# Performance work log

Measured on AMD Instinct MI355X. Metric: run time of the kernel, lower is better.

## Reference

```python
import jax, jax.numpy as jnp
import numpy as np

NUM_HEADS = 16
QKV = 1024
OUT = 1024
HEAD_DIM = QKV // NUM_HEADS


def _rel_shift(x):
    # x: [b,h,q,k] -> Transformer-XL relative shift
    zero_pad = jnp.zeros(x.shape[:-1] + (1,), dtype=x.dtype)
    x_padded = jnp.concatenate([zero_pad, x], axis=-1)
    x_padded = x_padded.reshape(x.shape[:-2] + (x.shape[-1] + 1, x.shape[-2]))
    return x_padded[..., 1:, :].reshape(x.shape)


def setup_inputs() -> dict:
    key = jax.random.key(0)
    ks = jax.random.split(key, 12)
    B, Q, K, D = 2, 2048, 2048, 1024
    s = 0.02
    return {
        "inputs_kv": jax.random.normal(ks[0], (B, K, D), jnp.float32),
        "inputs_q": jax.random.normal(ks[1], (B, Q, D), jnp.float32),
        "pos_embed": jax.random.normal(ks[2], (K, D), jnp.float32),
        "Wq_w": jax.random.normal(ks[3], (D, QKV), jnp.float32) * s,
        "Wq_b": jnp.zeros((QKV,), jnp.float32),
        "Wk_w": jax.random.normal(ks[4], (D, QKV), jnp.float32) * s,
        "Wk_b": jnp.zeros((QKV,), jnp.float32),
        "Wv_w": jax.random.normal(ks[5], (D, QKV), jnp.float32) * s,
        "Wv_b": jnp.zeros((QKV,), jnp.float32),
        "Wr_w": jax.random.normal(ks[6], (D, QKV), jnp.float32) * s,  # no bias
        "r_w_bias": jax.random.normal(ks[7], (NUM_HEADS, HEAD_DIM), jnp.float32) * s,
        "r_r_bias": jax.random.normal(ks[8], (NUM_HEADS, HEAD_DIM), jnp.float32) * s,
        "Wo_w": jax.random.normal(ks[9], (QKV, OUT), jnp.float32) * s,
        "Wo_b": jnp.zeros((OUT,), jnp.float32),
    }


def reference(inputs_kv, inputs_q, pos_embed, Wq_w, Wq_b, Wk_w, Wk_b, Wv_w, Wv_b,
              Wr_w, r_w_bias, r_r_bias, Wo_w, Wo_b):
    B, Q, _ = inputs_q.shape
    K = inputs_kv.shape[1]
    H, hd = NUM_HEADS, HEAD_DIM
    scale = hd ** (-0.5)

    q = (inputs_q @ Wq_w + Wq_b).reshape(B, Q, H, hd)
    k = (inputs_kv @ Wk_w + Wk_b).reshape(B, K, H, hd)
    v = (inputs_kv @ Wv_w + Wv_b).reshape(B, K, H, hd)
    r = (pos_embed @ Wr_w).reshape(K, H, hd)

    # content bias: [b,h,1,k]; position bias: [b,h,q,k] with rel-shift
    content_bias = jnp.einsum('hd,bkhd->bhk', r_w_bias, k)[:, :, None, :] * scale
    position_bias = jnp.einsum('bqhd,khd->bhqk', q + r_r_bias, r) * scale
    position_bias = _rel_shift(position_bias)
    combined_bias = content_bias + position_bias

    # dot_product_attention with extra bias and scale
    scores = jnp.einsum('bqhd,bkhd->bhqk', q, k) * scale + combined_bias
    probs = jax.nn.softmax(scores, axis=-1)
    out = jnp.einsum('bhqk,bkhd->bqhd', probs, v)

    out = out.reshape(B, Q, H * hd)
    return out @ Wo_w + Wo_b
```

## Files before the change

kernel.cpp:

```cpp
#include <hip/hip_runtime.h>
#include <hip/hip_fp16.h>


typedef float  floatx4 __attribute__((ext_vector_type(4)));
typedef __bf16 bf16x8  __attribute__((ext_vector_type(8)));
typedef _Float16 f16x8 __attribute__((ext_vector_type(8)));
typedef _Float16 f16x4 __attribute__((ext_vector_type(4)));
typedef _Float16 f16x2 __attribute__((ext_vector_type(2)));

#define LSTR 40
#define SCL 0.18033688f

struct GP {
  const void* A;
  const __bf16* B;
  int lda, ldb, K;
  float* outF;
  __bf16* out1;
  const float* bias;
};

__global__ void __launch_bounds__(256) gemm_o(GP p) {
  __shared__ __align__(16) __bf16 lA[128 * 32];
  __shared__ __align__(16) __bf16 lB[128 * 32];
  const int t = threadIdx.x;
  const int wave = t >> 6, lane = t & 63;
  const int m0 = blockIdx.y * 128, n0 = blockIdx.x * 128;
  const __bf16* Ab = (const __bf16*)p.A;
  const __bf16* Bb = p.B;

  floatx4 acc[4][4];
#pragma unroll
  for (int i = 0; i < 4; i++)
#pragma unroll
    for (int j = 0; j < 4; j++) acc[i][j] = floatx4{0.f, 0.f, 0.f, 0.f};

  const int lr = lane & 15, lq = lane >> 4;
  const int wr = (wave >> 1) << 6, wc = (wave & 1) << 6;

  for (int kk = 0; kk < 1024; kk += 32) {
#pragma unroll
    for (int i = 0; i < 2; i++) {
      const int idx = (i << 8) + t;
      const int row = idx >> 2, ch = (idx & 3) << 3;
      *(bf16x8*)&lA[row * 32 + ch] = *(const bf16x8*)(Ab + (long)(m0 + row) * 1024 + kk + ch);
      *(bf16x8*)&lB[row * 32 + ch] = *(const bf16x8*)(Bb + (long)(n0 + row) * 1024 + kk + ch);
    }
    __syncthreads();
    bf16x8 aF[4], bF[4];
#pragma unroll
    for (int i = 0; i < 4; i++)
      aF[i] = *(bf16x8*)&lA[(wr + i * 16 + lr) * 32 + (lq << 3)];
#pragma unroll
    for (int i = 0; i < 4; i++)
      bF[i] = *(bf16x8*)&lB[(wc + i * 16 + lr) * 32 + (lq << 3)];
#pragma unroll
    for (int i = 0; i < 4; i++)
#pragma unroll
      for (int j = 0; j < 4; j++)
        acc[i][j] = __builtin_amdgcn_mfma_f32_16x16x32_bf16(aF[i], bF[j], acc[i][j], 0, 0, 0);
    __syncthreads();
  }
#pragma unroll
  for (int i = 0; i < 4; i++)
#pragma unroll
    for (int j = 0; j < 4; j++) {
      int col = n0 + wc + j * 16 + lr;
#pragma unroll
      for (int g = 0; g < 4; g++) {
        int rl = m0 + wr + i * 16 + (lq << 2) + g;
        p.outF[(long)rl * 1024 + col] = acc[i][j][g] + p.bias[col];
      }
    }
}

struct QPAll {
  const float *qin, *kvin, *pos;
  const __bf16 *qinb, *kvinb, *posb;
  const __bf16 *Wtq, *Wtk, *Wtv, *Wtr;
  const float *bq, *bk, *bv, *rrb;
  __bf16 *qb, *qrr, *kb, *rb;
  _Float16 *vt;
};

template<bool BF16A>
__global__ void __launch_bounds__(256) qkvr_k(QPAll p) {
  constexpr int AST = BF16A ? 32 : LSTR;
  __shared__ __align__(16) __bf16 lA[128 * AST];
  __shared__ __align__(16) __bf16 lB[128 * AST];
  const int jb = blockIdx.x;
  const int job = (jb >= 768) ? 3 : (jb >> 8);
  const int local = jb - ((job == 3) ? 768 : (job << 8));
  const int m0 = (local >> 3) * 128, n0 = (local & 7) * 128;

  const float* Af; const __bf16* Ab; const __bf16* B; const float* bias;
  if (job == 0)      { Af = p.qin;  Ab = p.qinb;  B = p.Wtq; bias = p.bq; }
  else if (job == 1) { Af = p.kvin; Ab = p.kvinb; B = p.Wtk; bias = p.bk; }
  else if (job == 2) { Af = p.kvin; Ab = p.kvinb; B = p.Wtv; bias = p.bv; }
  else               { Af = p.pos;  Ab = p.posb;  B = p.Wtr; bias = nullptr; }

  const int t = threadIdx.x;
  const int wave = t >> 6, lane = t & 63;
  const int srow = t >> 2, scol = (t & 3) << 3;

  floatx4 acc[4][4];
#pragma unroll
  for (int i = 0; i < 4; i++)
#pragma unroll
    for (int j = 0; j < 4; j++) acc[i][j] = floatx4{0.f, 0.f, 0.f, 0.f};

  const int lr = lane & 15, lq = lane >> 4;
  const int wr = (wave >> 1) << 6, wc = (wave & 1) << 6;

  for (int kk = 0; kk < 1024; kk += 32) {
    if constexpr (BF16A) {
#pragma unroll
      for (int i = 0; i < 2; i++) {
        const int idx = (i << 8) + t;
        const int row = idx >> 2, ch = (idx & 3) << 3;
        *(bf16x8*)&lA[row * 32 + ch] = *(const bf16x8*)(Ab + (long)(m0 + row) * 1024 + kk + ch);
        *(bf16x8*)&lB[row * 32 + ch] = *(const bf16x8*)(B + (long)(n0 + row) * 1024 + kk + ch);
      }
    } else {
#pragma unroll
      for (int h2 = 0; h2 < 2; h2++) {
        int r = srow + (h2 << 6);
        const float* ap = Af + (long)(m0 + r) * 1024 + kk + scol;
        float4 f0 = *(const float4*)ap;
        float4 f1 = *(const float4*)(ap + 4);
        bf16x8 o;
        o[0] = (__bf16)f0.x; o[1] = (__bf16)f0.y; o[2] = (__bf16)f0.z; o[3] = (__bf16)f0.w;
        o[4] = (__bf16)f1.x; o[5] = (__bf16)f1.y; o[6] = (__bf16)f1.z; o[7] = (__bf16)f1.w;
        *(bf16x8*)&lA[r * AST + scol] = o;
        const __bf16* bp = B + (long)(n0 + r) * 1024 + kk + scol;
        *(bf16x8*)&lB[r * AST + scol] = *(const bf16x8*)bp;
      }
    }
    __syncthreads();
    bf16x8 aF[4], bF[4];
#pragma unroll
    for (int i = 0; i < 4; i++)
      aF[i] = *(bf16x8*)&lA[(wr + i * 16 + lr) * AST + (lq << 3)];
#pragma unroll
    for (int i = 0; i < 4; i++)
      bF[i] = *(bf16x8*)&lB[(wc + i * 16 + lr) * AST + (lq << 3)];
#pragma unroll
    for (int i = 0; i < 4; i++)
#pragma unroll
      for (int j = 0; j < 4; j++)
        acc[i][j] = __builtin_amdgcn_mfma_f32_16x16x32_bf16(aF[i], bF[j], acc[i][j], 0, 0, 0);
    __syncthreads();
  }

#pragma unroll
  for (int i = 0; i < 4; i++)
#pragma unroll
    for (int j = 0; j < 4; j++) {
      int col = n0 + wc + j * 16 + lr;
#pragma unroll
      for (int g = 0; g < 4; g++) {
        int rl = m0 + wr + i * 16 + (lq << 2) + g;
        float val = acc[i][j][g];
        int hh = col >> 6, d = col & 63;
        if (job == 3) {
          long dst = (((long)hh * 2048 + rl) << 6) + d;
          p.rb[dst] = (__bf16)val;
        } else {
          int bb = rl >> 11, s = rl & 2047;
          float v = val + bias[col];
          if (job == 0) {
            long dst = (((long)(bb * 16 + hh) * 2048 + s) << 6) + d;
            p.qb[dst] = (__bf16)v;
            p.qrr[dst] = (__bf16)(v + p.rrb[col]);
          } else if (job == 1) {
            long dst = (((long)(bb * 16 + hh) * 2048 + s) << 6) + d;
            p.kb[dst] = (__bf16)v;
          } else {
            long dst = ((((long)(bb * 16 + hh)) << 6) + d) * 2048 + s;
            p.vt[dst] = (_Float16)v;
          }
        }
      }
    }
}

__global__ void __launch_bounds__(256) cb_k(const __bf16* kb, const float* rwb, float* cb) {
  long id = (long)blockIdx.x * 256 + threadIdx.x;
  int z = (int)(id >> 11);
  int j = (int)(id & 2047);
  int h = z & 15;
  const __bf16* kp = kb + (((long)z * 2048 + j) << 6);
  float s = 0.f;
#pragma unroll
  for (int c = 0; c < 8; c++) {
    bf16x8 kv = *(const bf16x8*)(kp + c * 8);
#pragma unroll
    for (int e = 0; e < 8; e++) s += rwb[h * 64 + c * 8 + e] * (float)kv[e];
  }
  cb[id] = s * SCL;
}

struct TRP {
  const float* src[5]; __bf16* dst[5];
  const float* csrc[3]; __bf16* cdst[3]; long clen[3];
};
__global__ void __launch_bounds__(256) tr_cvt_all(TRP p) {
  const int id = blockIdx.x;
  if (id >= 1280) {
    const int cj = (id - 1280) >> 8;
    const int cbk = (id - 1280) & 255;
    const float* s = p.csrc[cj];
    __bf16* d = p.cdst[cj];
    const long n = p.clen[cj];
    for (long i = ((long)cbk * 256 + threadIdx.x) * 8; i < n; i += (long)256 * 256 * 8) {
      float4 f0 = *(const float4*)(s + i);
      float4 f1 = *(const float4*)(s + i + 4);
      bf16x8 o;
      o[0] = (__bf16)f0.x; o[1] = (__bf16)f0.y; o[2] = (__bf16)f0.z; o[3] = (__bf16)f0.w;
      o[4] = (__bf16)f1.x; o[5] = (__bf16)f1.y; o[6] = (__bf16)f1.z; o[7] = (__bf16)f1.w;
      *(bf16x8*)(d + i) = o;
    }
    return;
  }
  __shared__ float tile[64][65];
  const int which = id >> 8;
  const int local = id & 255;
  const int bx = local & 15, by = local >> 4;
  const float* src = p.src[which];
  __bf16* dst = p.dst[which];
  int tx = threadIdx.x & 63, ty = threadIdx.x >> 6;
#pragma unroll
  for (int r = ty; r < 64; r += 4)
    tile[r][tx] = src[(long)(by * 64 + r) * 1024 + bx * 64 + tx];
  __syncthreads();
#pragma unroll
  for (int r = ty; r < 64; r += 4)
    dst[(long)(bx * 64 + r) * 1024 + by * 64 + tx] = (__bf16)tile[tx][r];
}

#define QW 256
#define QSTR3 264
#define SM_ONE (32 * QSTR3 * 2)
#define FUSED_SMEM (2 * SM_ONE + 2048)

__global__ void __launch_bounds__(256, 4) fused_k(const __bf16* __restrict__ qb,
                                                  const __bf16* __restrict__ qrr,
                                                  const __bf16* __restrict__ kb,
                                                  const _Float16* __restrict__ vt,
                                                  const __bf16* __restrict__ rb,
                                                  const float* __restrict__ cb,
                                                  __bf16* __restrict__ attnb) {
  extern __shared__ char smem[];
  _Float16* qkS = (_Float16*)smem;
  _Float16* xS  = (_Float16*)(smem + SM_ONE);
  _Float16* xB  = (_Float16*)(smem + 2 * SM_ONE);
  __shared__ float sInv[32];

  const int t = threadIdx.x;
  const int w = t >> 6, lane = t & 63, lr = lane & 15, lq = lane >> 4;
  const int obid = blockIdx.x;
  const int bid = ((obid & 7) << 8) | (obid >> 3);
  const int z  = bid >> 6;
  const int i0 = (bid & 63) << 5;
  const int b = z >> 4, h = z & 15;
  const bool early = (i0 <= 1023);
  const int astart = early ? i0 + 1 : i0;
  const int grow = early ? 0 : 31;
  const int c0   = early ? 0 : i0 + 33;

  bf16x8 fq[2][2], fr[2][2];
#pragma unroll
  for (int rg2 = 0; rg2 < 2; rg2++) {
    const __bf16* qp = qb + (((long)z * 2048 + i0 + rg2 * 16 + lr) << 6) + lq * 8;
    fq[rg2][0] = *(const bf16x8*)qp; fq[rg2][1] = *(const bf16x8*)(qp + 32);
    const __bf16* rp = qrr + (((long)z * 2048 + astart + rg2 * 16 + lr) << 6) + lq * 8;
    fr[rg2][0] = *(const bf16x8*)rp; fr[rg2][1] = *(const bf16x8*)(rp + 32);
  }

  const __bf16* kbz = kb + (((long)z * 2048) << 6);
  const __bf16* rbh = rb + (((long)h * 2048) << 6);
  const float* cbz = cb + (long)z * 2048;
  const _Float16* vtz = vt + (((long)z) << 6) * 2048;

  {
    const int ga    = early ? i0 : i0 + 32;
    const int m0g   = early ? (2047 - i0) : 0;
    int ncols = early ? (i0 + 1) : (2015 - i0);
    if (ncols < 0) ncols = 0;
    const int dl = (t & 7) << 3;
    bf16x8 qv = *(const bf16x8*)(qrr + (((long)z * 2048 + ga) << 6) + dl);
    for (int c = t >> 3; c < ncols; c += 32) {
      bf16x8 rv = *(const bf16x8*)(rbh + ((long)(m0g + c) << 6) + dl);
      float s = 0.f;
#pragma unroll
      for (int e = 0; e < 8; e++) s += (float)qv[e] * (float)rv[e];
      s += __shfl_xor(s, 1, 64);
      s += __shfl_xor(s, 2, 64);
      s += __shfl_xor(s, 4, 64);
      if ((t & 7) == 0) xB[c] = (_Float16)(s * SCL);
    }
  }
  __syncthreads();

  const int erow = w * 8 + (lane >> 3);
  const int ecol = (lane & 7) * 16;
  const int rg = w >> 1, sl = w & 1;

  floatx4 oacc[4];
#pragma unroll
  for (int s = 0; s < 4; s++) oacc[s] = floatx4{0.f, 0.f, 0.f, 0.f};
  float psum = 0.f;

  for (int kp = 0; kp < 8; kp++) {
    const int J0 = kp << 8;

#pragma unroll
    for (int s = 0; s < 4; s++) {
      const int jt = ((w << 2) + s) << 4;
      const __bf16* ap = kbz + ((long)(J0 + jt + lr) << 6) + lq * 8;
      bf16x8 a0 = *(const bf16x8*)ap, a1 = *(const bf16x8*)(ap + 32);
      floatx4 cbv = *(const floatx4*)(cbz + J0 + jt + lq * 4);
      floatx4 c0v{0.f, 0.f, 0.f, 0.f}, c1v{0.f, 0.f, 0.f, 0.f};
      c0v = __builtin_amdgcn_mfma_f32_16x16x32_bf16(a0, fq[0][0], c0v, 0, 0, 0);
      c0v = __builtin_amdgcn_mfma_f32_16x16x32_bf16(a1, fq[0][1], c0v, 0, 0, 0);
      c1v = __builtin_amdgcn_mfma_f32_16x16x32_bf16(a0, fq[1][0], c1v, 0, 0, 0);
      c1v = __builtin_amdgcn_mfma_f32_16x16x32_bf16(a1, fq[1][1], c1v, 0, 0, 0);
      f16x4 s0v, s1v;
#pragma unroll
      for (int g = 0; g < 4; g++) {
        s0v[g] = (_Float16)(c0v[g] * SCL + cbv[g]);
        s1v[g] = (_Float16)(c1v[g] * SCL + cbv[g]);
      }
      *(f16x4*)&qkS[lr * QSTR3 + jt + lq * 4] = s0v;
      *(f16x4*)&qkS[(16 + lr) * QSTR3 + jt + lq * 4] = s1v;
    }

    const int mb = ((J0 - astart - 32) & 2047) & ~15;
#pragma unroll
    for (int s = 0; s < 5; s++) {
      const int mt = w + (s << 2);
      if (mt < 19) {
        const int m0 = (mb + (mt << 4)) & 2047;
        const __bf16* rp2 = rbh + ((long)(m0 + lr) << 6) + lq * 8;
        bf16x8 r0 = *(const bf16x8*)rp2, r1 = *(const bf16x8*)(rp2 + 32);
        floatx4 x0{0.f, 0.f, 0.f, 0.f}, x1{0.f, 0.f, 0.f, 0.f};
        x0 = __builtin_amdgcn_mfma_f32_16x16x32_bf16(r0, fr[0][0], x0, 0, 0, 0);
        x0 = __builtin_amdgcn_mfma_f32_16x16x32_bf16(r1, fr[0][1], x0, 0, 0, 0);
        x1 = __builtin_amdgcn_mfma_f32_16x16x32_bf16(r0, fr[1][0], x1, 0, 0, 0);
        x1 = __builtin_amdgcn_mfma_f32_16x16x32_bf16(r1, fr[1][1], x1, 0, 0, 0);
#pragma unroll
        for (int rg2 = 0; rg2 < 2; rg2++) {
          const int a = astart + (rg2 << 4) + lr;
          const floatx4 ax = rg2 ? x1 : x0;
#pragma unroll
          for (int g = 0; g < 4; g++) {
            const int m = m0 + (lq << 2) + g;
            const int sum = m + a + 1;
            const int j = sum & 2047;
            const int ri = (sum >= 2048) ? (a - i0) : (a - i0 - 1);
            const int jl = j - J0;
            if ((unsigned)ri < 32u && (unsigned)jl < (unsigned)QW)
              xS[ri * QSTR3 + jl] = (_Float16)(ax[g] * SCL);
          }
        }
      }
    }

    {
      const int j = J0 + t;
      const bool act = early ? (j <= i0) : (j >= c0);
      if (act) xS[grow * QSTR3 + t] = xB[j - c0];
    }
    if (t < 32) {
      const int jl = i0 + t + 1 - J0;
      if ((unsigned)jl < (unsigned)QW) xS[t * QSTR3 + jl] = (_Float16)0.f;
    }
    __syncthreads();

    {
      _Float16* qrow = qkS + erow * QSTR3;
      const _Float16* xrow = xS + erow * QSTR3;
      const f16x2 one2 = {(_Float16)1.f, (_Float16)1.f};
#pragma unroll
      for (int ii = 0; ii < 2; ii++) {
        const int cbase = ii * 128 + ecol;
        f16x8 h0 = *(const f16x8*)(qrow + cbase), h1 = *(const f16x8*)(qrow + cbase + 8);
        f16x8 v0 = *(const f16x8*)(xrow + cbase), v1 = *(const f16x8*)(xrow + cbase + 8);
        f16x8 s0 = h0 + v0, s1 = h1 + v1;
        f16x8 p0, p1;
#pragma unroll
        for (int e2 = 0; e2 < 4; e2++) {
          __half2 a2, b2;
          __builtin_memcpy(&a2, (const char*)&s0 + e2 * 4, 4);
          a2 = h2exp2(a2);
          __builtin_memcpy((char*)&p0 + e2 * 4, &a2, 4);
          f16x2 af2; __builtin_memcpy(&af2, &a2, 4);
          psum = __builtin_amdgcn_fdot2(af2, one2, psum, false);
          __builtin_memcpy(&b2, (const char*)&s1 + e2 * 4, 4);
          b2 = h2exp2(b2);
          __builtin_memcpy((char*)&p1 + e2 * 4, &b2, 4);
          f16x2 bf2; __builtin_memcpy(&bf2, &b2, 4);
          psum = __builtin_amdgcn_fdot2(bf2, one2, psum, false);
        }
        *(f16x8*)(qrow + cbase) = p0;
        *(f16x8*)(qrow + cbase + 8) = p1;
      }
    }
    __syncthreads();

#pragma unroll
    for (int ch = 0; ch < 4; ch++) {
      const int kk = sl * 128 + ch * 32;
      f16x8 af = *(const f16x8*)(qkS + (rg * 16 + lr) * QSTR3 + kk + lq * 8);
#pragma unroll
      for (int sub = 0; sub < 4; sub++) {
        f16x8 bfv = *(const f16x8*)(vtz + (long)(sub * 16 + lr) * 2048 + J0 + kk + lq * 8);
        oacc[sub] = __builtin_amdgcn_mfma_f32_16x16x32_f16(af, bfv, oacc[sub], 0, 0, 0);
      }
    }
    __syncthreads();
  }

  {
    float* sPart = (float*)smem;
#pragma unroll
    for (int sub = 0; sub < 4; sub++)
#pragma unroll
      for (int g = 0; g < 4; g++)
        sPart[((rg << 1) + sl) * 1024 + ((lq << 2) + g) * 64 + sub * 16 + lr] = oacc[sub][g];
  }
#pragma unroll
  for (int o = 1; o < 8; o <<= 1) psum += __shfl_xor(psum, o, 64);
  if ((lane & 7) == 0) sInv[erow] = 1.0f / psum;
  __syncthreads();

  {
    const float* sPart = (const float*)smem;
    const int r = t >> 3, d0 = (t & 7) << 3;
    const int rg2 = r >> 4, rl = r & 15;
    const float inv = sInv[r];
    bf16x8 ov;
#pragma unroll
    for (int e = 0; e < 8; e++) {
      float acc = sPart[(rg2 << 1) * 1024 + rl * 64 + d0 + e] +
                  sPart[((rg2 << 1) + 1) * 1024 + rl * 64 + d0 + e];
      ov[e] = (__bf16)(acc * inv);
    }
    *(bf16x8*)&attnb[((long)b * 2048 + i0 + r) * 1024 + h * 64 + d0] = ov;
  }
}

extern "C" void kernel_launch(void* const* d_in, const int* in_sizes, int n_in,
                              void* d_out, int out_size, void* d_ws, size_t ws_size,
                              hipStream_t stream) {
  (void)in_sizes; (void)n_in; (void)out_size;
  const float* inputs_kv = (const float*)d_in[0];
  const float* inputs_q  = (const float*)d_in[1];
  const float* pos_embed = (const float*)d_in[2];
  const float* Wq_w = (const float*)d_in[3];
  const float* Wq_b = (const float*)d_in[4];
  const float* Wk_w = (const float*)d_in[5];
  const float* Wk_b = (const float*)d_in[6];
  const float* Wv_w = (const float*)d_in[7];
  const float* Wv_b = (const float*)d_in[8];
  const float* Wr_w = (const float*)d_in[9];
  const float* rwb  = (const float*)d_in[10];
  const float* rrb  = (const float*)d_in[11];
  const float* Wo_w = (const float*)d_in[12];
  const float* Wo_b = (const float*)d_in[13];

  char* ws = (char*)d_ws;
  const long MB = 1 << 20;
  __bf16* Wtq = (__bf16*)(ws + 0 * MB);
  __bf16* Wtk = (__bf16*)(ws + 2 * MB);
  __bf16* Wtv = (__bf16*)(ws + 4 * MB);
  __bf16* Wtr = (__bf16*)(ws + 6 * MB);
  __bf16* Wto = (__bf16*)(ws + 8 * MB);
  __bf16* qb  = (__bf16*)(ws + 10 * MB);
  __bf16* qrr = (__bf16*)(ws + 18 * MB);
  __bf16* kb  = (__bf16*)(ws + 26 * MB);
  _Float16* vt = (_Float16*)(ws + 34 * MB);
  __bf16* rb  = (__bf16*)(ws + 42 * MB);
  float*  cb  = (float*)(ws + 46 * MB);
  __bf16* attnb = (__bf16*)(ws + 47 * MB);
  __bf16* qinb  = (__bf16*)(ws + 55 * MB);
  __bf16* kvinb = (__bf16*)(ws + 63 * MB);
  __bf16* posb  = (__bf16*)(ws + 71 * MB);
  const bool big = ws_size >= (size_t)(76 * MB);

  dim3 blk(256);

  TRP tp{};
  tp.src[0] = Wq_w; tp.dst[0] = Wtq;
  tp.src[1] = Wk_w; tp.dst[1] = Wtk;
  tp.src[2] = Wv_w; tp.dst[2] = Wtv;
  tp.src[3] = Wr_w; tp.dst[3] = Wtr;
  tp.src[4] = Wo_w; tp.dst[4] = Wto;
  tp.csrc[0] = inputs_q;  tp.cdst[0] = qinb;  tp.clen[0] = 4096L * 1024;
  tp.csrc[1] = inputs_kv; tp.cdst[1] = kvinb; tp.clen[1] = 4096L * 1024;
  tp.csrc[2] = pos_embed; tp.cdst[2] = posb;  tp.clen[2] = 2048L * 1024;
  tr_cvt_all<<<dim3(big ? 2048 : 1280), blk, 0, stream>>>(tp);

  QPAll q{};
  q.qin = inputs_q; q.kvin = inputs_kv; q.pos = pos_embed;
  q.qinb = qinb; q.kvinb = kvinb; q.posb = posb;
  q.Wtq = Wtq; q.Wtk = Wtk; q.Wtv = Wtv; q.Wtr = Wtr;
  q.bq = Wq_b; q.bk = Wk_b; q.bv = Wv_b; q.rrb = rrb;
  q.qb = qb; q.qrr = qrr; q.kb = kb; q.rb = rb; q.vt = vt;
  if (big) qkvr_k<true><<<dim3(896), blk, 0, stream>>>(q);
  else     qkvr_k<false><<<dim3(896), blk, 0, stream>>>(q);

  cb_k<<<dim3(256), blk, 0, stream>>>(kb, rwb, cb);

  fused_k<<<dim3(2048), dim3(256), FUSED_SMEM, stream>>>(qb, qrr, kb, vt, rb, cb, attnb);

  GP o{};
  o.A = attnb; o.B = Wto; o.lda = 1024; o.ldb = 1024; o.K = 1024;
  o.bias = Wo_b; o.outF = (float*)d_out;
  gemm_o<<<dim3(8, 32), blk, 0, stream>>>(o);
}
```

Measured before the change: 510.3 us.

## Shrink workspace: reuse attn buffer for q bf16, skip pos conversion, halve output GEMM M-tile

Removes the separate bf16 copy of pos_embed, so the R projection converts fp32 to bf16 inline. The bf16 inputs_q copy is aliased onto the attention output buffer, which lowers the workspace threshold for the pre-converted path. The query job always reads pre-converted bf16 A, and the padded LDS stride is used for every job. The output GEMM drops to a 64-row M tile, doubling its block count for better CU occupancy at the cost of less B-tile reuse.

```diff
diff --git a/kernel.cpp b/kernel.cpp
--- a/kernel.cpp
+++ b/kernel.cpp
@@ -21,48 +21,51 @@
 };
 
 __global__ void __launch_bounds__(256) gemm_o(GP p) {
-  __shared__ __align__(16) __bf16 lA[128 * 32];
+  __shared__ __align__(16) __bf16 lA[64 * 32];
   __shared__ __align__(16) __bf16 lB[128 * 32];
   const int t = threadIdx.x;
   const int wave = t >> 6, lane = t & 63;
-  const int m0 = blockIdx.y * 128, n0 = blockIdx.x * 128;
+  const int m0 = blockIdx.y * 64, n0 = blockIdx.x * 128;
   const __bf16* Ab = (const __bf16*)p.A;
   const __bf16* Bb = p.B;
 
-  floatx4 acc[4][4];
-#pragma unroll
-  for (int i = 0; i < 4; i++)
+  floatx4 acc[2][4];
+#pragma unroll
+  for (int i = 0; i < 2; i++)
 #pragma unroll
     for (int j = 0; j < 4; j++) acc[i][j] = floatx4{0.f, 0.f, 0.f, 0.f};
 
   const int lr = lane & 15, lq = lane >> 4;
-  const int wr = (wave >> 1) << 6, wc = (wave & 1) << 6;
+  const int wr = (wave >> 1) << 5, wc = (wave & 1) << 6;
 
   for (int kk = 0; kk < 1024; kk += 32) {
+    {
+      const int row = t >> 2, ch = (t & 3) << 3;
+      *(bf16x8*)&lA[row * 32 + ch] = *(const bf16x8*)(Ab + (long)(m0 + row) * 1024 + kk + ch);
+    }
 #pragma unroll
     for (int i = 0; i < 2; i++) {
       const int idx = (i << 8) + t;
       const int row = idx >> 2, ch = (idx & 3) << 3;
-      *(bf16x8*)&lA[row * 32 + ch] = *(const bf16x8*)(Ab + (long)(m0 + row) * 1024 + kk + ch);
       *(bf16x8*)&lB[row * 32 + ch] = *(const bf16x8*)(Bb + (long)(n0 + row) * 1024 + kk + ch);
     }
     __syncthreads();
-    bf16x8 aF[4], bF[4];
-#pragma unroll
-    for (int i = 0; i < 4; i++)
+    bf16x8 aF[2], bF[4];
+#pragma unroll
+    for (int i = 0; i < 2; i++)
       aF[i] = *(bf16x8*)&lA[(wr + i * 16 + lr) * 32 + (lq << 3)];
 #pragma unroll
-    for (int i = 0; i < 4; i++)
-      bF[i] = *(bf16x8*)&lB[(wc + i * 16 + lr) * 32 + (lq << 3)];
-#pragma unroll
-    for (int i = 0; i < 4; i++)
+    for (int j = 0; j < 4; j++)
+      bF[j] = *(bf16x8*)&lB[(wc + j * 16 + lr) * 32 + (lq << 3)];
+#pragma unroll
+    for (int i = 0; i < 2; i++)
 #pragma unroll
       for (int j = 0; j < 4; j++)
         acc[i][j] = __builtin_amdgcn_mfma_f32_16x16x32_bf16(aF[i], bF[j], acc[i][j], 0, 0, 0);
     __syncthreads();
   }
 #pragma unroll
-  for (int i = 0; i < 4; i++)
+  for (int i = 0; i < 2; i++)
 #pragma unroll
     for (int j = 0; j < 4; j++) {
       int col = n0 + wc + j * 16 + lr;
@@ -76,32 +79,31 @@
 
 struct QPAll {
   const float *qin, *kvin, *pos;
-  const __bf16 *qinb, *kvinb, *posb;
+  const __bf16 *qinb, *kvinb;
   const __bf16 *Wtq, *Wtk, *Wtv, *Wtr;
   const float *bq, *bk, *bv, *rrb;
   __bf16 *qb, *qrr, *kb, *rb;
   _Float16 *vt;
 };
 
-template<bool BF16A>
 __global__ void __launch_bounds__(256) qkvr_k(QPAll p) {
-  constexpr int AST = BF16A ? 32 : LSTR;
-  __shared__ __align__(16) __bf16 lA[128 * AST];
-  __shared__ __align__(16) __bf16 lB[128 * AST];
+  __shared__ __align__(16) __bf16 lA[128 * LSTR];
+  __shared__ __align__(16) __bf16 lB[128 * LSTR];
   const int jb = blockIdx.x;
   const int job = (jb >= 768) ? 3 : (jb >> 8);
   const int local = jb - ((job == 3) ? 768 : (job << 8));
   const int m0 = (local >> 3) * 128, n0 = (local & 7) * 128;
 
-  const float* Af; const __bf16* Ab; const __bf16* B; const float* bias;
-  if (job == 0)      { Af = p.qin;  Ab = p.qinb;  B = p.Wtq; bias = p.bq; }
-  else if (job == 1) { Af = p.kvin; Ab = p.kvinb; B = p.Wtk; bias = p.bk; }
-  else if (job == 2) { Af = p.kvin; Ab = p.kvinb; B = p.Wtv; bias = p.bv; }
-  else               { Af = p.pos;  Ab = p.posb;  B = p.Wtr; bias = nullptr; }
+  const float* Af = nullptr; const __bf16* Ab = nullptr;
+  const __bf16* B; const float* bias;
+  if (job == 0)      { Ab = p.qinb;  B = p.Wtq; bias = p.bq; }
+  else if (job == 1) { Ab = p.kvinb; Af = p.kvin; B = p.Wtk; bias = p.bk; }
+  else if (job == 2) { Ab = p.kvinb; Af = p.kvin; B = p.Wtv; bias = p.bv; }
+  else               { Af = p.pos;   B = p.Wtr; bias = nullptr; }
+  const bool abf16 = (Ab != nullptr);
 
   const int t = threadIdx.x;
   const int wave = t >> 6, lane = t & 63;
-  const int srow = t >> 2, scol = (t & 3) << 3;
 
   floatx4 acc[4][4];
 #pragma unroll
@@ -113,37 +115,31 @@
   const int wr = (wave >> 1) << 6, wc = (wave & 1) << 6;
 
   for (int kk = 0; kk < 1024; kk += 32) {
-    if constexpr (BF16A) {
-#pragma unroll
-      for (int i = 0; i < 2; i++) {
-        const int idx = (i << 8) + t;
-        const int row = idx >> 2, ch = (idx & 3) << 3;
-        *(bf16x8*)&lA[row * 32 + ch] = *(const bf16x8*)(Ab + (long)(m0 + row) * 1024 + kk + ch);
-        *(bf16x8*)&lB[row * 32 + ch] = *(const bf16x8*)(B + (long)(n0 + row) * 1024 + kk + ch);
-      }
-    } else {
-#pragma unroll
-      for (int h2 = 0; h2 < 2; h2++) {
-        int r = srow + (h2 << 6);
-        const float* ap = Af + (long)(m0 + r) * 1024 + kk + scol;
+#pragma unroll
+    for (int i = 0; i < 2; i++) {
+      const int idx = (i << 8) + t;
+      const int row = idx >> 2, ch = (idx & 3) << 3;
+      if (abf16) {
+        *(bf16x8*)&lA[row * LSTR + ch] = *(const bf16x8*)(Ab + (long)(m0 + row) * 1024 + kk + ch);
+      } else {
+        const float* ap = Af + (long)(m0 + row) * 1024 + kk + ch;
         float4 f0 = *(const float4*)ap;
         float4 f1 = *(const float4*)(ap + 4);
         bf16x8 o;
         o[0] = (__bf16)f0.x; o[1] = (__bf16)f0.y; o[2] = (__bf16)f0.z; o[3] = (__bf16)f0.w;
         o[4] = (__bf16)f1.x; o[5] = (__bf16)f1.y; o[6] = (__bf16)f1.z; o[7] = (__bf16)f1.w;
-        *(bf16x8*)&lA[r * AST + scol] = o;
-        const __bf16* bp = B + (long)(n0 + r) * 1024 + kk + scol;
-        *(bf16x8*)&lB[r * AST + scol] = *(const bf16x8*)bp;
-      }
+        *(bf16x8*)&lA[row * LSTR + ch] = o;
+      }
+      *(bf16x8*)&lB[row * LSTR + ch] = *(const bf16x8*)(B + (long)(n0 + row) * 1024 + kk + ch);
     }
     __syncthreads();
     bf16x8 aF[4], bF[4];
 #pragma unroll
     for (int i = 0; i < 4; i++)
-      aF[i] = *(bf16x8*)&lA[(wr + i * 16 + lr) * AST + (lq << 3)];
+      aF[i] = *(bf16x8*)&lA[(wr + i * 16 + lr) * LSTR + (lq << 3)];
 #pragma unroll
     for (int i = 0; i < 4; i++)
-      bF[i] = *(bf16x8*)&lB[(wc + i * 16 + lr) * AST + (lq << 3)];
+      bF[i] = *(bf16x8*)&lB[(wc + i * 16 + lr) * LSTR + (lq << 3)];
 #pragma unroll
     for (int i = 0; i < 4; i++)
 #pragma unroll
@@ -202,7 +198,7 @@
 
 struct TRP {
   const float* src[5]; __bf16* dst[5];
-  const float* csrc[3]; __bf16* cdst[3]; long clen[3];
+  const float* csrc[2]; __bf16* cdst[2]; long clen[2];
 };
 __global__ void __launch_bounds__(256) tr_cvt_all(TRP p) {
   const int id = blockIdx.x;
@@ -483,10 +479,9 @@
   __bf16* rb  = (__bf16*)(ws + 42 * MB);
   float*  cb  = (float*)(ws + 46 * MB);
   __bf16* attnb = (__bf16*)(ws + 47 * MB);
-  __bf16* qinb  = (__bf16*)(ws + 55 * MB);
-  __bf16* kvinb = (__bf16*)(ws + 63 * MB);
-  __bf16* posb  = (__bf16*)(ws + 71 * MB);
-  const bool big = ws_size >= (size_t)(76 * MB);
+  __bf16* qinb  = attnb;
+  __bf16* kvinb = (__bf16*)(ws + 55 * MB);
+  const bool big1 = ws_size >= (size_t)(63 * MB);
 
   dim3 blk(256);
 
@@ -498,17 +493,15 @@
   tp.src[4] = Wo_w; tp.dst[4] = Wto;
   tp.csrc[0] = inputs_q;  tp.cdst[0] = qinb;  tp.clen[0] = 4096L * 1024;
   tp.csrc[1] = inputs_kv; tp.cdst[1] = kvinb; tp.clen[1] = 4096L * 1024;
-  tp.csrc[2] = pos_embed; tp.cdst[2] = posb;  tp.clen[2] = 2048L * 1024;
-  tr_cvt_all<<<dim3(big ? 2048 : 1280), blk, 0, stream>>>(tp);
+  tr_cvt_all<<<dim3(big1 ? 1792 : 1536), blk, 0, stream>>>(tp);
 
   QPAll q{};
   q.qin = inputs_q; q.kvin = inputs_kv; q.pos = pos_embed;
-  q.qinb = qinb; q.kvinb = kvinb; q.posb = posb;
+  q.qinb = qinb; q.kvinb = big1 ? kvinb : nullptr;
   q.Wtq = Wtq; q.Wtk = Wtk; q.Wtv = Wtv; q.Wtr = Wtr;
   q.bq = Wq_b; q.bk = Wk_b; q.bv = Wv_b; q.rrb = rrb;
   q.qb = qb; q.qrr = qrr; q.kb = kb; q.rb = rb; q.vt = vt;
-  if (big) qkvr_k<true><<<dim3(896), blk, 0, stream>>>(q);
-  else     qkvr_k<false><<<dim3(896), blk, 0, stream>>>(q);
+  qkvr_k<<<dim3(896), blk, 0, stream>>>(q);
 
   cb_k<<<dim3(256), blk, 0, stream>>>(kb, rwb, cb);
 
@@ -517,5 +510,5 @@
   GP o{};
   o.A = attnb; o.B = Wto; o.lda = 1024; o.ldb = 1024; o.K = 1024;
   o.bias = Wo_b; o.outF = (float*)d_out;
-  gemm_o<<<dim3(8, 32), blk, 0, stream>>>(o);
+  gemm_o<<<dim3(8, 64), blk, 0, stream>>>(o);
 }
```

New measurement: 523.3 us. +2.6%, slower.
